# Kernel optimization log

Measured on AMD Instinct MI355X. Metric: run time of the kernel, lower is better.

## Reference

```python
import jax, jax.numpy as jnp
import numpy as np

# Dims / scalars (from init_kwargs: m = int(T/dt), delta = dt, theta_star = threshold)
M = 50000
N = 500
DELTA = 0.001
GLEAK = 1.0
TAUS = 10.0
THETA_STAR = 1.0
SPIKE_PROB = 0.02  # sparse binary spike raster as produced by time2spike


def setup_inputs() -> dict:
    key = jax.random.key(0)
    k1, k2, k3 = jax.random.split(key, 3)
    # binary spike raster [m, n]
    spikes = (jax.random.uniform(k1, (M, N)) < SPIKE_PROB).astype(jnp.float32)
    # synapse weights ~ N(w_mean=0.01, 0.01)
    w = (0.01 + 0.01 * jax.random.normal(k2, (N,))).astype(jnp.float32)
    # reversal potentials: half excitatory (ex=5), half inhibitory (inh=-1), shuffled
    vrev = jnp.where(jax.random.uniform(k3, (N,)) < 0.5, 5.0, -1.0).astype(jnp.float32)
    return {"spikes": spikes, "w": w, "vrev": vrev}


def reference(spikes, w, vrev):
    dtype = spikes.dtype
    decay = jnp.exp(jnp.asarray(-1.0 / TAUS, dtype))

    # _compute_exp: exp_temp[i] = (exp_temp[i-1] + spikes[i-1]) * exp(-1/taus), exp_temp[0] = 0
    def exp_step(carry, s):
        nxt = (carry + s) * decay
        return nxt, nxt

    _, e_tail = jax.lax.scan(exp_step, jnp.zeros((N,), dtype), spikes[:-1])
    exp_temp = jnp.concatenate([jnp.zeros((1, N), dtype), e_tail], axis=0)  # [M, N]

    # Gsyn_pre = |w| * exp_temp ; Isyn_pre = Vrev * |w| * exp_temp.
    # Only their per-timestep sums over synapses enter the vtr recurrence,
    # so contract over n immediately instead of materializing [M, N] products.
    absw = jnp.abs(w)
    g_sum = exp_temp @ absw            # [M] = sum_j Gsyn_pre[i, j]
    i_sum = exp_temp @ (vrev * absw)   # [M] = sum_j Isyn_pre[i, j]
    a = DELTA * (GLEAK + g_sum)        # per-step leak+conductance factor
    b = DELTA * i_sum                  # per-step input drive

    # _computevtr: if vtr[i-1] < theta: vtr[i] = vtr[i-1]*(1 - a[i-1]) + b[i-1]
    # else vtr[i] stays 0 (state reset after threshold crossing), vtr[0] = 0.
    def vtr_step(v, ab):
        ai, bi = ab
        nxt = jnp.where(v < THETA_STAR, v * (1.0 - ai) + bi, jnp.asarray(0.0, dtype))
        return nxt, nxt

    _, v_tail = jax.lax.scan(vtr_step, jnp.asarray(0.0, dtype), (a[:-1], b[:-1]))
    vtr = jnp.concatenate([jnp.zeros((1,), dtype), v_tail])  # [M]
    return vtr
```

## Files before the change

kernel.cpp:

```cpp
#include <hip/hip_runtime.h>
#include <hip/hip_cooperative_groups.h>
#include <cmath>

namespace cg = cooperative_groups;

namespace {
constexpr int NELEM  = 50000;
constexpr int NSYN   = 500;
constexpr int NQ4    = 125;
constexpr int T      = 1024;
constexpr int SBLK   = 49;
constexpr int SLOTS  = SBLK * T;
constexpr int CMAXC  = (NELEM - 1) >> 6;
constexpr int NCH_PAD = 784;
constexpr int MAXSEG = 4096;
constexpr int NGRP   = NELEM / 8;
constexpr double DELTA_D = 1.0e-3;
constexpr double THETA_D = 1.0;
constexpr float  DECAY_F = 0.90483741803595957311f;
}

struct WS {
    double2 rq[SLOTS];
    double  gAm[64], gAg[64], gAi[64];
    double  gPp[64], gPq[64];
    double  gmaxR[1024];
    double  gbndQ[MAXSEG];
    int     gbnd[MAXSEG];
    int     gnseg;
    int     pad;
    float   swv[SLOTS];
    float   iwv[SLOTS];
};

__global__ __launch_bounds__(256) void k_rowdot(
    const float* __restrict__ spikes,
    const float* __restrict__ w,
    const float* __restrict__ vrev,
    float* __restrict__ swv,
    float* __restrict__ iwv)
{
    const int lane = threadIdx.x & 63;
    const int wv   = threadIdx.x >> 6;
    const int rg   = blockIdx.x * 4 + wv;
    if (rg >= NGRP) return;
    const int row0 = rg * 8;

    const float4* __restrict__ w4 = reinterpret_cast<const float4*>(w);
    const float4* __restrict__ r4 = reinterpret_cast<const float4*>(vrev);
    const int j1 = lane;
    const int j2 = lane + 64;
    const bool has2 = (j2 < NQ4);
    float4 a1 = w4[j1], r1 = r4[j1];
    float4 aw1 = make_float4(fabsf(a1.x), fabsf(a1.y), fabsf(a1.z), fabsf(a1.w));
    float4 ar1 = make_float4(aw1.x * r1.x, aw1.y * r1.y, aw1.z * r1.z, aw1.w * r1.w);
    float4 aw2 = make_float4(0.f, 0.f, 0.f, 0.f), ar2 = aw2;
    if (has2) {
        float4 a2 = w4[j2], r2 = r4[j2];
        aw2 = make_float4(fabsf(a2.x), fabsf(a2.y), fabsf(a2.z), fabsf(a2.w));
        ar2 = make_float4(aw2.x * r2.x, aw2.y * r2.y, aw2.z * r2.z, aw2.w * r2.w);
    }

    float sp[8], ip[8];
#pragma unroll
    for (int r = 0; r < 8; ++r) {
        const float4* __restrict__ srow =
            reinterpret_cast<const float4*>(spikes + (size_t)(row0 + r) * NSYN);
        float4 s1 = srow[j1];
        float a = s1.x * aw1.x + s1.y * aw1.y + s1.z * aw1.z + s1.w * aw1.w;
        float b = s1.x * ar1.x + s1.y * ar1.y + s1.z * ar1.z + s1.w * ar1.w;
        if (has2) {
            float4 s2 = srow[j2];
            a += s2.x * aw2.x + s2.y * aw2.y + s2.z * aw2.z + s2.w * aw2.w;
            b += s2.x * ar2.x + s2.y * ar2.y + s2.z * ar2.z + s2.w * ar2.w;
        }
        sp[r] = a; ip[r] = b;
    }
#pragma unroll
    for (int d = 32; d > 0; d >>= 1) {
#pragma unroll
        for (int r = 0; r < 8; ++r) {
            sp[r] += __shfl_xor(sp[r], d);
            ip[r] += __shfl_xor(ip[r], d);
        }
    }
    if (lane == 0) {
        *reinterpret_cast<float4*>(swv + row0)     = make_float4(sp[0], sp[1], sp[2], sp[3]);
        *reinterpret_cast<float4*>(swv + row0 + 4) = make_float4(sp[4], sp[5], sp[6], sp[7]);
        *reinterpret_cast<float4*>(iwv + row0)     = make_float4(ip[0], ip[1], ip[2], ip[3]);
        *reinterpret_cast<float4*>(iwv + row0 + 4) = make_float4(ip[4], ip[5], ip[6], ip[7]);
    }
}

__global__ __launch_bounds__(1024) void k_fused(WS* __restrict__ ws, float* __restrict__ out)
{
    cg::grid_group grid = cg::this_grid();
    const int tid = threadIdx.x, lane = tid & 63, wv = tid >> 6, blk = blockIdx.x;
    const int idx = blk * T + tid;
    const bool live = (idx < NELEM);
    const double decay = (double)DECAY_F;

    __shared__ double s_a[16], s_b[16], s_c[16];
    __shared__ double s_qg0, s_qi0, s_qp0, s_qq0;
    __shared__ double smax[NCH_PAD];
    __shared__ int    sb[MAXSEG];
    __shared__ double sq[MAXSEG];
    __shared__ int    s_nseg;

    double s = live ? (double)ws->swv[idx] : 0.0;
    double t = live ? (double)ws->iwv[idx] : 0.0;
    double m_in = live ? decay : 1.0;
    double g_in = live ? s * decay : 0.0;
    double i_in = live ? t * decay : 0.0;
#pragma unroll
    for (int d = 1; d < 64; d <<= 1) {
        double pm = __shfl_up(m_in, d);
        double pg = __shfl_up(g_in, d);
        double pi = __shfl_up(i_in, d);
        if (lane >= d) {
            g_in = m_in * pg + g_in;
            i_in = m_in * pi + i_in;
            m_in = pm * m_in;
        }
    }
    if (lane == 63) { s_a[wv] = m_in; s_b[wv] = g_in; s_c[wv] = i_in; }
    __syncthreads();
    if (wv == 0) {
        double wm = (lane < 16) ? s_a[lane] : 1.0;
        double wg = (lane < 16) ? s_b[lane] : 0.0;
        double wi = (lane < 16) ? s_c[lane] : 0.0;
#pragma unroll
        for (int d = 1; d < 16; d <<= 1) {
            double pm = __shfl_up(wm, d);
            double pg = __shfl_up(wg, d);
            double pi = __shfl_up(wi, d);
            if (lane >= d) {
                wg = wm * pg + wg;
                wi = wm * pi + wi;
                wm = pm * wm;
            }
        }
        if (lane < 16) { s_a[lane] = wm; s_b[lane] = wg; s_c[lane] = wi; }
        if (lane == 15) { ws->gAm[blk] = wm; ws->gAg[blk] = wg; ws->gAi[blk] = wi; }
    }
    __syncthreads();
    double em = __shfl_up(m_in, 1), eg = __shfl_up(g_in, 1), ei = __shfl_up(i_in, 1);
    if (lane == 0) { em = 1.0; eg = 0.0; ei = 0.0; }
    if (wv > 0) {
        double qm = s_a[wv - 1], qg = s_b[wv - 1], qi = s_c[wv - 1];
        eg = em * qg + eg;
        ei = em * qi + ei;
        em = qm * em;
    }

    grid.sync();

    if (wv == 0) {
        double am = (lane < SBLK) ? ws->gAm[lane] : 1.0;
        double ag = (lane < SBLK) ? ws->gAg[lane] : 0.0;
        double ai = (lane < SBLK) ? ws->gAi[lane] : 0.0;
#pragma unroll
        for (int d = 1; d < 64; d <<= 1) {
            double pm = __shfl_up(am, d);
            double pg = __shfl_up(ag, d);
            double pi = __shfl_up(ai, d);
            if (lane >= d) {
                ag = am * pg + ag;
                ai = am * pi + ai;
                am = pm * am;
            }
        }
        double zg = __shfl_up(ag, 1), zi = __shfl_up(ai, 1);
        if (lane == 0) { zg = 0.0; zi = 0.0; }
        if (lane == blk) { s_qg0 = zg; s_qi0 = zi; }
    }
    __syncthreads();

    double Eg = em * s_qg0 + eg;
    double Ei = em * s_qi0 + ei;
    double p_in = 1.0, q_in = 0.0;
    if (live) {
        double aa = DELTA_D * (1.0 + Eg);
        double om = 1.0 - aa;
        p_in = om;
        q_in = (DELTA_D * Ei) / om;
    }
#pragma unroll
    for (int d = 1; d < 64; d <<= 1) {
        double pp = __shfl_up(p_in, d);
        double pq = __shfl_up(q_in, d);
        if (lane >= d) {
            q_in = pq + q_in / pp;
            p_in = pp * p_in;
        }
    }
    if (lane == 63) { s_a[wv] = p_in; s_b[wv] = q_in; }
    __syncthreads();
    if (wv == 0) {
        double wp = (lane < 16) ? s_a[lane] : 1.0;
        double wq = (lane < 16) ? s_b[lane] : 0.0;
#pragma unroll
        for (int d = 1; d < 16; d <<= 1) {
            double pp = __shfl_up(wp, d);
            double pq = __shfl_up(wq, d);
            if (lane >= d) {
                wq = pq + wq / pp;
                wp = pp * wp;
            }
        }
        if (lane < 16) { s_a[lane] = wp; s_b[lane] = wq; }
        if (lane == 15) { ws->gPp[blk] = wp; ws->gPq[blk] = wq; }
    }
    __syncthreads();
    double ep = __shfl_up(p_in, 1), eq = __shfl_up(q_in, 1);
    if (lane == 0) { ep = 1.0; eq = 0.0; }
    if (wv > 0) {
        double ap2 = s_a[wv - 1], aq2 = s_b[wv - 1];
        eq = aq2 + eq / ap2;
        ep = ap2 * ep;
    }

    grid.sync();

    if (wv == 0) {
        double ap = (lane < SBLK) ? ws->gPp[lane] : 1.0;
        double aq = (lane < SBLK) ? ws->gPq[lane] : 0.0;
#pragma unroll
        for (int d = 1; d < 64; d <<= 1) {
            double pp = __shfl_up(ap, d);
            double pq = __shfl_up(aq, d);
            if (lane >= d) {
                aq = pq + aq / pp;
                ap = pp * ap;
            }
        }
        double zp = __shfl_up(ap, 1), zq = __shfl_up(aq, 1);
        if (lane == 0) { zp = 1.0; zq = 0.0; }
        if (lane == blk) { s_qp0 = zp; s_qq0 = zq; }
    }
    __syncthreads();
    double Q = s_qq0 + eq / s_qp0;
    double P = s_qp0 * ep;
    double R = live ? (Q - THETA_D / P) : -1.0e308;
    ws->rq[idx] = make_double2(R, Q);
    double mR = R;
#pragma unroll
    for (int d = 32; d > 0; d >>= 1) mR = fmax(mR, __shfl_xor(mR, d));
    if (lane == 0) ws->gmaxR[idx >> 6] = mR;

    grid.sync();

    if (blk == 0) {
        for (int c = tid; c < NCH_PAD; c += T)
            smax[c] = (c <= CMAXC) ? ws->gmaxR[c] : -1.0e308;
        __syncthreads();
        if (tid < 64) {
            int nseg = 1;
            if (lane == 0) { ws->gbnd[0] = 0; ws->gbndQ[0] = 0.0; }
            double Qr = 0.0;
            int pos = 1;
            while (pos < NELEM && nseg < MAXSEG) {
                int c = pos >> 6;
                int i0 = -1;
                double Qnb = 0.0;
                while (true) {
                    int cf = -1;
                    for (int cb = c; cb <= CMAXC; cb += 64) {
                        int cc = cb + lane;
                        bool qy = (cc <= CMAXC) && (smax[cc] >= Qr);
                        unsigned long long m = __ballot(qy);
                        if (m) { cf = cb + __builtin_ctzll(m); break; }
                    }
                    if (cf < 0) break;
                    int i = (cf << 6) + lane;
                    bool valid = (i >= pos) && (i < NELEM);
                    double2 rv = valid ? ws->rq[i] : make_double2(-1.0e308, 0.0);
                    unsigned long long m2 = __ballot(valid && (rv.x >= Qr));
                    if (m2) {
                        int r = __builtin_ctzll(m2);
                        i0 = (cf << 6) + r;
                        if (r < 63) Qnb = __shfl(rv.y, r + 1);
                        break;
                    }
                    c = cf + 1;
                    if (c > CMAXC) break;
                }
                if (i0 < 0) break;
                int nb = i0 + 1;
                if (nb >= NELEM) break;
                if ((i0 & 63) == 63) Qnb = ws->rq[nb].y;
                Qr = Qnb;
                if (lane == 0) { ws->gbnd[nseg] = nb; ws->gbndQ[nseg] = Qr; }
                nseg++;
                pos = nb + 1;
            }
            if (lane == 0) ws->gnseg = nseg;
        } else {
            double acc = 0.0;
            for (int i = tid; i < NELEM; i += 7 * T) acc += ws->rq[i].x;
            asm volatile("" :: "v"((float)acc));
        }
    } else if ((blk & 7) == 0) {
        const int p = blk >> 3;
        double acc = 0.0;
        for (int i = p * T + tid; i < NELEM; i += 7 * T) acc += ws->rq[i].x;
        asm volatile("" :: "v"((float)acc));
    }

    grid.sync();

    if (tid == 0) s_nseg = ws->gnseg;
    __syncthreads();
    const int nseg = s_nseg;
    for (int i2 = tid; i2 < nseg; i2 += T) { sb[i2] = ws->gbnd[i2]; sq[i2] = ws->gbndQ[i2]; }
    __syncthreads();
    if (live) {
        int lo = 0, hi = nseg - 1;
        while (lo < hi) {
            int mid = (lo + hi + 1) >> 1;
            if (sb[mid] <= idx) lo = mid; else hi = mid - 1;
        }
        out[idx] = (idx == sb[lo]) ? 0.0f : (float)(P * (Q - sq[lo]));
    }
}

extern "C" void kernel_launch(void* const* d_in, const int* in_sizes, int n_in,
                              void* d_out, int out_size, void* d_ws, size_t ws_size,
                              hipStream_t stream) {
    const float* spikes = (const float*)d_in[0];
    const float* w      = (const float*)d_in[1];
    const float* vrev   = (const float*)d_in[2];
    float* out = (float*)d_out;
    WS* ws = (WS*)d_ws;

    hipLaunchKernelGGL(k_rowdot, dim3((NGRP + 3) / 4), dim3(256), 0, stream,
                       spikes, w, vrev, ws->swv, ws->iwv);

    WS* wsp = ws; float* outp = out;
    void* args[2] = { (void*)&wsp, (void*)&outp };
    (void)hipLaunchCooperativeKernel((const void*)k_fused, dim3(SBLK), dim3(T),
                                     args, 0, stream);
}
```

Baseline: 234.2 us.

## Split cooperative fused kernel into separate stream-ordered kernels instead of grid syncs

```diff
diff --git a/kernel.cpp b/kernel.cpp
--- a/kernel.cpp
+++ b/kernel.cpp
@@ -1,8 +1,5 @@
 #include <hip/hip_runtime.h>
-#include <hip/hip_cooperative_groups.h>
 #include <cmath>
-
-namespace cg = cooperative_groups;
 
 namespace {
 constexpr int NELEM  = 50000;
@@ -22,6 +19,8 @@
 
 struct WS {
     double2 rq[SLOTS];
+    double  eAm[SLOTS], eAg[SLOTS], eAi[SLOTS];
+    double  ePl[SLOTS], eQl[SLOTS];
     double  gAm[64], gAg[64], gAi[64];
     double  gPp[64], gPq[64];
     double  gmaxR[1024];
@@ -92,23 +91,18 @@
     }
 }
 
-__global__ __launch_bounds__(1024) void k_fused(WS* __restrict__ ws, float* __restrict__ out)
-{
-    cg::grid_group grid = cg::this_grid();
+__global__ __launch_bounds__(1024) void k_scanA(const float* __restrict__ swv,
+                                                const float* __restrict__ iwv,
+                                                WS* __restrict__ ws)
+{
     const int tid = threadIdx.x, lane = tid & 63, wv = tid >> 6, blk = blockIdx.x;
     const int idx = blk * T + tid;
     const bool live = (idx < NELEM);
     const double decay = (double)DECAY_F;
-
     __shared__ double s_a[16], s_b[16], s_c[16];
-    __shared__ double s_qg0, s_qi0, s_qp0, s_qq0;
-    __shared__ double smax[NCH_PAD];
-    __shared__ int    sb[MAXSEG];
-    __shared__ double sq[MAXSEG];
-    __shared__ int    s_nseg;
-
-    double s = live ? (double)ws->swv[idx] : 0.0;
-    double t = live ? (double)ws->iwv[idx] : 0.0;
+
+    double s = live ? (double)swv[idx] : 0.0;
+    double t = live ? (double)iwv[idx] : 0.0;
     double m_in = live ? decay : 1.0;
     double g_in = live ? s * decay : 0.0;
     double i_in = live ? t * decay : 0.0;
@@ -152,8 +146,18 @@
         ei = em * qi + ei;
         em = qm * em;
     }
-
-    grid.sync();
+    ws->eAm[idx] = em; ws->eAg[idx] = eg; ws->eAi[idx] = ei;
+}
+
+__global__ __launch_bounds__(1024) void k_scanB(WS* __restrict__ ws)
+{
+    const int tid = threadIdx.x, lane = tid & 63, wv = tid >> 6, blk = blockIdx.x;
+    const int idx = blk * T + tid;
+    const bool live = (idx < NELEM);
+    __shared__ double s_a[16], s_b[16];
+    __shared__ double s_qg0, s_qi0;
+
+    double em = ws->eAm[idx], eg = ws->eAg[idx], ei = ws->eAi[idx];
 
     if (wv == 0) {
         double am = (lane < SBLK) ? ws->gAm[lane] : 1.0;
@@ -215,12 +219,21 @@
     double ep = __shfl_up(p_in, 1), eq = __shfl_up(q_in, 1);
     if (lane == 0) { ep = 1.0; eq = 0.0; }
     if (wv > 0) {
-        double ap2 = s_a[wv - 1], aq2 = s_b[wv - 1];
-        eq = aq2 + eq / ap2;
-        ep = ap2 * ep;
-    }
-
-    grid.sync();
+        double ap = s_a[wv - 1], aq = s_b[wv - 1];
+        eq = aq + eq / ap;
+        ep = ap * ep;
+    }
+    ws->ePl[idx] = ep; ws->eQl[idx] = eq;
+}
+
+__global__ __launch_bounds__(1024) void k_apply(WS* __restrict__ ws)
+{
+    const int tid = threadIdx.x, lane = tid & 63, wv = tid >> 6, blk = blockIdx.x;
+    const int idx = blk * T + tid;
+    const bool live = (idx < NELEM);
+    __shared__ double s_qp0, s_qq0;
+
+    double pl = ws->ePl[idx], ql = ws->eQl[idx];
 
     if (wv == 0) {
         double ap = (lane < SBLK) ? ws->gPp[lane] : 1.0;
@@ -239,22 +252,29 @@
         if (lane == blk) { s_qp0 = zp; s_qq0 = zq; }
     }
     __syncthreads();
-    double Q = s_qq0 + eq / s_qp0;
-    double P = s_qp0 * ep;
+
+    double Q = s_qq0 + ql / s_qp0;
+    double P = s_qp0 * pl;
     double R = live ? (Q - THETA_D / P) : -1.0e308;
     ws->rq[idx] = make_double2(R, Q);
     double mR = R;
 #pragma unroll
     for (int d = 32; d > 0; d >>= 1) mR = fmax(mR, __shfl_xor(mR, d));
     if (lane == 0) ws->gmaxR[idx >> 6] = mR;
-
-    grid.sync();
+}
+
+__global__ __launch_bounds__(1024) void k_search(WS* __restrict__ ws)
+{
+    const int tid = threadIdx.x, blk = blockIdx.x;
 
     if (blk == 0) {
+        __shared__ double smax[NCH_PAD];
         for (int c = tid; c < NCH_PAD; c += T)
             smax[c] = (c <= CMAXC) ? ws->gmaxR[c] : -1.0e308;
         __syncthreads();
+
         if (tid < 64) {
+            const int lane = tid;
             int nseg = 1;
             if (lane == 0) { ws->gbnd[0] = 0; ws->gbndQ[0] = 0.0; }
             double Qr = 0.0;
@@ -306,21 +326,35 @@
         for (int i = p * T + tid; i < NELEM; i += 7 * T) acc += ws->rq[i].x;
         asm volatile("" :: "v"((float)acc));
     }
-
-    grid.sync();
-
+}
+
+__global__ __launch_bounds__(1024) void k_fill(const WS* __restrict__ ws,
+                                               float* __restrict__ out)
+{
+    __shared__ int    sb[MAXSEG];
+    __shared__ double sq[MAXSEG];
+    __shared__ int    s_nseg;
+    const int tid = threadIdx.x;
     if (tid == 0) s_nseg = ws->gnseg;
     __syncthreads();
     const int nseg = s_nseg;
-    for (int i2 = tid; i2 < nseg; i2 += T) { sb[i2] = ws->gbnd[i2]; sq[i2] = ws->gbndQ[i2]; }
-    __syncthreads();
-    if (live) {
+    for (int i = tid; i < nseg; i += T) { sb[i] = ws->gbnd[i]; sq[i] = ws->gbndQ[i]; }
+    __syncthreads();
+
+    const int idx = blockIdx.x * T + tid;
+    if (idx < NELEM) {
         int lo = 0, hi = nseg - 1;
         while (lo < hi) {
             int mid = (lo + hi + 1) >> 1;
             if (sb[mid] <= idx) lo = mid; else hi = mid - 1;
         }
-        out[idx] = (idx == sb[lo]) ? 0.0f : (float)(P * (Q - sq[lo]));
+        if (idx == sb[lo]) {
+            out[idx] = 0.0f;
+        } else {
+            double2 v = ws->rq[idx];
+            double P = THETA_D / (v.y - v.x);
+            out[idx] = (float)(P * (v.y - sq[lo]));
+        }
     }
 }
 
@@ -335,9 +369,9 @@
 
     hipLaunchKernelGGL(k_rowdot, dim3((NGRP + 3) / 4), dim3(256), 0, stream,
                        spikes, w, vrev, ws->swv, ws->iwv);
-
-    WS* wsp = ws; float* outp = out;
-    void* args[2] = { (void*)&wsp, (void*)&outp };
-    (void)hipLaunchCooperativeKernel((const void*)k_fused, dim3(SBLK), dim3(T),
-                                     args, 0, stream);
-}
+    hipLaunchKernelGGL(k_scanA,  dim3(SBLK), dim3(T), 0, stream, ws->swv, ws->iwv, ws);
+    hipLaunchKernelGGL(k_scanB,  dim3(SBLK), dim3(T), 0, stream, ws);
+    hipLaunchKernelGGL(k_apply,  dim3(SBLK), dim3(T), 0, stream, ws);
+    hipLaunchKernelGGL(k_search, dim3(56),   dim3(T), 0, stream, ws);
+    hipLaunchKernelGGL(k_fill,   dim3(SBLK), dim3(T), 0, stream, ws, out);
+}
```

New measurement: 197.0 us. 15.9% less time.
